# Performance work log

Hardware: AMD Instinct MI355X
Metric: run time of the kernel (lower is better)

Reference implementation:

```python
import jax, jax.numpy as jnp
import numpy as np

N = 100000
E = 1600000
IN_DIM = 128
OUT_DIM = 64


def setup_inputs() -> dict:
    key = jax.random.key(0)
    k_h, k_ei, k_ew, k_W, k_a = jax.random.split(key, 5)
    h = jax.random.normal(k_h, (N, IN_DIM), dtype=jnp.float32)
    edge_index = jax.random.randint(k_ei, (2, E), 0, N, dtype=jnp.int64)
    edge_weight = jax.random.uniform(k_ew, (E,), dtype=jnp.float32)
    # nn.Linear weights (Kaiming-uniform-ish scale)
    W = jax.random.uniform(k_W, (OUT_DIM, IN_DIM), dtype=jnp.float32,
                           minval=-1.0, maxval=1.0) / np.sqrt(IN_DIM)
    a = jax.random.uniform(k_a, (2 * OUT_DIM,), dtype=jnp.float32,
                           minval=-1.0, maxval=1.0) / np.sqrt(2 * OUT_DIM)
    return {"h": h, "edge_index": edge_index, "edge_weight": edge_weight,
            "W": W, "a": a}


def reference(h, edge_index, edge_weight, W, a):
    # Faithful translation of _GATConvSparse.forward (inference; dropout = identity).
    n = h.shape[0]
    src, dst = edge_index[0], edge_index[1]
    Wh = h @ W.T                                  # (N, out_dim)
    d = Wh.shape[1]
    # a(cat([Wh[src], Wh[dst]])) == Wh[src] @ a[:d] + Wh[dst] @ a[d:]
    alpha = Wh[src] @ a[:d] + Wh[dst] @ a[d:]     # (E,)
    alpha = alpha * edge_weight
    # Buggy-but-faithful 'softmax': segment-sum raw scores onto dst nodes...
    alpha_node = jax.ops.segment_sum(alpha, dst, num_segments=n)   # (N,)
    alpha_exp = jnp.exp(alpha_node - alpha_node.max())             # (N,)
    # ...then normalize per-edge exp(src) by sum of exp(src) over each dst segment.
    denom = jax.ops.segment_sum(alpha_exp[src], dst, num_segments=n)  # (N,)
    alpha_norm = alpha_exp[src] / (denom[dst] + 1e-9)              # (E,)
    out = jax.ops.segment_sum(alpha_norm[:, None] * Wh[src], dst,
                              num_segments=n)                      # (N, out_dim)
    return jax.nn.elu(out)
```

## Files before the change

### kernel.cpp

```cpp
#include <hip/hip_runtime.h>
#include <math.h>

#define Nn 100000
#define Ee 1600000
#define IND 128
#define OUTD 64
#define DPB 64
#define NB 1563
#define CAP 1536
#define GB 1563
#define EB_BLOCKS 391
#define AFIX 1048576.0f

using bf16x8 = __attribute__((ext_vector_type(8))) short;
using f32x4 = __attribute__((ext_vector_type(4))) float;

__device__ __forceinline__ unsigned short f2bf(float f) {
    unsigned u = __float_as_uint(f);
    u = u + 0x7FFFu + ((u >> 16) & 1u);
    return (unsigned short)(u >> 16);
}
__device__ __forceinline__ float bf2f(unsigned short h) {
    return __uint_as_float(((unsigned)h) << 16);
}

__device__ __forceinline__ bool probe64(const void* __restrict__ ei) {
    const long long* p = (const long long*)ei;
    bool ok = true;
#pragma unroll
    for (int i = 0; i < 8; ++i) {
        long long v = p[i];
        ok = ok && (v >= 0 && v < Nn);
    }
    return ok;
}

__device__ __forceinline__ void load_edge(const void* ei, int e, bool is64,
                                          int& s, int& d) {
    if (is64) {
        const long long* p = (const long long*)ei;
        s = (int)p[e];
        d = (int)p[Ee + e];
    } else {
        const int* p = (const int*)ei;
        s = p[e];
        d = p[Ee + e];
    }
}

__device__ __forceinline__ int load_dst(const void* ei, int e, bool is64) {
    if (is64) return (int)((const long long*)ei)[Ee + e];
    return ((const int*)ei)[Ee + e];
}

__global__ __launch_bounds__(256) void k_fused(
    const float* __restrict__ h, const float* __restrict__ W,
    const float* __restrict__ a, unsigned short* __restrict__ Whb,
    float* __restrict__ s1, float* __restrict__ s2,
    const void* __restrict__ ei, int* __restrict__ bcount) {
    __shared__ unsigned short Ash[64][136];
    __shared__ unsigned short Wsh[64][136];
    __shared__ float al[2 * OUTD];
    int bid = blockIdx.x;
    int t = threadIdx.x;

    if (bid < GB) {
        int R = bid * 64;
        for (int i = t; i < 2048; i += 256) {
            float4 v = ((const float4*)W)[i];
            int r = i >> 5, c = (i & 31) << 2;
            unsigned lo = (unsigned)f2bf(v.x) | ((unsigned)f2bf(v.y) << 16);
            unsigned hi = (unsigned)f2bf(v.z) | ((unsigned)f2bf(v.w) << 16);
            *(uint2*)&Wsh[r][c] = make_uint2(lo, hi);
        }
        if (t < 32) ((float4*)al)[t] = ((const float4*)a)[t];
        for (int i = t; i < 2048; i += 256) {
            int r = i >> 5, c = (i & 31) << 2;
            int n = R + r;
            float4 v = make_float4(0.f, 0.f, 0.f, 0.f);
            if (n < Nn) v = ((const float4*)(h + (size_t)n * IND))[i & 31];
            unsigned lo = (unsigned)f2bf(v.x) | ((unsigned)f2bf(v.y) << 16);
            unsigned hi = (unsigned)f2bf(v.z) | ((unsigned)f2bf(v.w) << 16);
            *(uint2*)&Ash[r][c] = make_uint2(lo, hi);
        }
        __syncthreads();

        int w = t >> 6, l = t & 63;
        int li = l & 15, lg = l >> 4;
        f32x4 acc[4];
#pragma unroll
        for (int nt = 0; nt < 4; ++nt) acc[nt] = (f32x4){0.f, 0.f, 0.f, 0.f};
#pragma unroll
        for (int kk = 0; kk < 4; ++kk) {
            bf16x8 af = *(const bf16x8*)&Ash[w * 16 + li][kk * 32 + lg * 8];
#pragma unroll
            for (int nt = 0; nt < 4; ++nt) {
                bf16x8 bf = *(const bf16x8*)&Wsh[nt * 16 + li][kk * 32 + lg * 8];
                acc[nt] = __builtin_amdgcn_mfma_f32_16x16x32_bf16(af, bf,
                                                                  acc[nt],
                                                                  0, 0, 0);
            }
        }
        float p1[4] = {0.f, 0.f, 0.f, 0.f};
        float p2[4] = {0.f, 0.f, 0.f, 0.f};
#pragma unroll
        for (int nt = 0; nt < 4; ++nt) {
            float a1v = al[nt * 16 + li];
            float a2v = al[OUTD + nt * 16 + li];
#pragma unroll
            for (int r = 0; r < 4; ++r) {
                float v = acc[nt][r];
                p1[r] += v * a1v;
                p2[r] += v * a2v;
                int row = R + w * 16 + lg * 4 + r;
                if (row < Nn)
                    Whb[(size_t)row * OUTD + nt * 16 + li] = f2bf(v);
            }
        }
#pragma unroll
        for (int r = 0; r < 4; ++r) {
#pragma unroll
            for (int m = 1; m < 16; m <<= 1) {
                p1[r] += __shfl_xor(p1[r], m, 64);
                p2[r] += __shfl_xor(p2[r], m, 64);
            }
        }
        if (li < 4) {
            int row = R + w * 16 + lg * 4 + li;
            if (row < Nn) {
                s1[row] = p1[li];
                s2[row] = p2[li];
            }
        }
    } else {
        int* cnt = (int*)&Ash[0][0];
        for (int i = t; i < NB; i += 256) cnt[i] = 0;
        __syncthreads();
        bool is64 = probe64(ei);
        int base = (bid - GB) * 4096;
#pragma unroll
        for (int i = 0; i < 16; ++i) {
            int e = base + i * 256 + t;
            if (e < Ee) atomicAdd(&cnt[load_dst(ei, e, is64) >> 6], 1);
        }
        __syncthreads();
        for (int i = t; i < NB; i += 256) {
            int c = cnt[i];
            if (c) atomicAdd(bcount + i, c);
        }
    }
}

__global__ __launch_bounds__(1024) void k_scan(
    const int* __restrict__ bcount, int* __restrict__ boff,
    int* __restrict__ bcursor) {
    __shared__ int sd[1024];
    int t = threadIdx.x;
    int i0 = 2 * t, i1 = 2 * t + 1;
    int v0 = (i0 < NB) ? bcount[i0] : 0;
    int v1 = (i1 < NB) ? bcount[i1] : 0;
    int pair = v0 + v1;
    sd[t] = pair;
    __syncthreads();
    for (int off = 1; off < 1024; off <<= 1) {
        int add = (t >= off) ? sd[t - off] : 0;
        __syncthreads();
        sd[t] += add;
        __syncthreads();
    }
    int excl = sd[t] - pair;
    if (i0 < NB) {
        boff[i0] = excl;
        bcursor[i0] = excl;
    }
    if (i1 < NB) {
        boff[i1] = excl + v0;
        bcursor[i1] = excl + v0;
    }
    if (t == 0) boff[NB] = Ee;
}

__global__ __launch_bounds__(512) void k_binscatter(
    const void* __restrict__ ei, const float* __restrict__ ew,
    const float* __restrict__ s1, const float* __restrict__ s2,
    int* __restrict__ bcursor, uint2* __restrict__ bins) {
    __shared__ int cnt[NB];
    __shared__ int gbase[NB];
    for (int i = threadIdx.x; i < NB; i += 512) cnt[i] = 0;
    __syncthreads();
    bool is64 = probe64(ei);
    int base = blockIdx.x * 4096;
    unsigned rx[8];
    int ryi[8];
    int rb[8];
    int rk[8];
#pragma unroll
    for (int i = 0; i < 8; ++i) {
        int e = base + i * 512 + threadIdx.x;
        rb[i] = -1;
        rx[i] = 0;
        ryi[i] = 0;
        rk[i] = 0;
        if (e < Ee) {
            int s, d;
            load_edge(ei, e, is64, s, d);
            float alpha = (s1[s] + s2[d]) * ew[e];
            ryi[i] = (int)rintf(alpha * AFIX);
            int b = d >> 6;
            rb[i] = b;
            rk[i] = atomicAdd(&cnt[b], 1);
            rx[i] = (unsigned)s | ((unsigned)(d & 63) << 17);
        }
    }
    __syncthreads();
    for (int i = threadIdx.x; i < NB; i += 512) {
        int c = cnt[i];
        if (c) gbase[i] = atomicAdd(bcursor + i, c);
    }
    __syncthreads();
#pragma unroll
    for (int i = 0; i < 8; ++i) {
        if (rb[i] >= 0) {
            bins[gbase[rb[i]] + rk[i]] = make_uint2(rx[i], (unsigned)ryi[i]);
        }
    }
}

__global__ __launch_bounds__(256) void k_balpha(
    const uint2* __restrict__ bins, const int* __restrict__ boff,
    float* __restrict__ ae) {
    __shared__ int anl[DPB];
    int b = blockIdx.x;
    int t = threadIdx.x;
    if (t < DPB) anl[t] = 0;
    __syncthreads();
    int e0 = boff[b], e1 = boff[b + 1];
    for (int k = e0 + t; k < e1; k += 256) {
        uint2 r = bins[k];
        atomicAdd(&anl[r.x >> 17], (int)r.y);
    }
    __syncthreads();
    if (t < DPB) {
        int n = b * DPB + t;
        if (n < Nn) ae[n] = expf((float)anl[t] * (1.f / AFIX));
    }
}

#define AGG_BODY(NR)                                                         \
    {                                                                        \
        uint2 rr[NR];                                                        \
        unsigned ww[NR];                                                     \
        _Pragma("unroll") for (int j = 0; j < NR; ++j)                       \
            rr[j] = lrec[k + 2 * j + half];                                  \
        _Pragma("unroll") for (int j = 0; j < NR; ++j)                       \
            ww[j] = whb32[(rr[j].x & 0x1FFFF) * 32 + hl];                    \
        _Pragma("unroll") for (int j = 0; j < NR; ++j) {                     \
            float aa = __uint_as_float(rr[j].y);                             \
            acc.x += aa * __uint_as_float(ww[j] << 16);                      \
            acc.y += aa * __uint_as_float(ww[j] & 0xFFFF0000u);              \
            den += aa;                                                       \
        }                                                                    \
    }

__global__ __launch_bounds__(512, 8) void k_agg(
    const uint2* __restrict__ bins, const int* __restrict__ boff,
    const float* __restrict__ ae, const unsigned short* __restrict__ Whb,
    float* __restrict__ out) {
    __shared__ uint2 lrec[CAP];
    __shared__ int cnt[DPB];
    __shared__ int sbase[DPB];
    int b = blockIdx.x;
    int t = threadIdx.x;
    int lane = t & 63;
    int wave = t >> 6;
    int half = lane >> 5;
    int hl = lane & 31;
    int e0 = boff[b], e1 = boff[b + 1];
    int total = e1 - e0;
    const unsigned* whb32 = (const unsigned*)Whb;

    if (t < DPB) cnt[t] = 0;
    __syncthreads();

    if (total <= CAP) {
        unsigned su[CAP / 512];
        float sa[CAP / 512];
        int srk[CAP / 512];
#pragma unroll
        for (int i = 0; i < CAP / 512; ++i) {
            int k = e0 + i * 512 + t;
            srk[i] = -1;
            su[i] = 0;
            sa[i] = 0.f;
            if (k < e1) {
                uint2 r = bins[k];
                srk[i] = atomicAdd(&cnt[r.x >> 17], 1);
                su[i] = r.x;
                sa[i] = ae[r.x & 0x1FFFF];
            }
        }
        __syncthreads();
        if (t < DPB) {
            int v = cnt[t];
#pragma unroll
            for (int d = 1; d < DPB; d <<= 1) {
                int u = __shfl_up(v, d, 64);
                if (t >= d) v += u;
            }
            sbase[t] = v;
        }
        __syncthreads();
#pragma unroll
        for (int i = 0; i < CAP / 512; ++i) {
            if (srk[i] >= 0) {
                int dloc = su[i] >> 17;
                int pos = sbase[dloc] - cnt[dloc] + srk[i];
                lrec[pos] = make_uint2(su[i], __float_as_uint(sa[i]));
            }
        }
        __syncthreads();

        for (int d = wave * 8; d < wave * 8 + 8; ++d) {
            int k1 = sbase[d];
            int k = k1 - cnt[d];
            float2 acc = make_float2(0.f, 0.f);
            float den = 0.f;
            for (; k + 15 < k1; k += 16) AGG_BODY(8);
            for (; k + 7 < k1; k += 8) AGG_BODY(4);
            for (; k + 1 < k1; k += 2) AGG_BODY(1);
            if (k < k1) {
                uint2 rA = lrec[k];
                unsigned wA = whb32[(rA.x & 0x1FFFF) * 32 + hl];
                float aA = half ? 0.f : __uint_as_float(rA.y);
                acc.x += aA * __uint_as_float(wA << 16);
                acc.y += aA * __uint_as_float(wA & 0xFFFF0000u);
                den += aA;
            }
            float ax = acc.x + __shfl_xor(acc.x, 32, 64);
            float ay = acc.y + __shfl_xor(acc.y, 32, 64);
            float dn = den + __shfl_xor(den, 32, 64);
            if (half == 0) {
                int n = b * DPB + d;
                if (n < Nn) {
                    float inv = 1.f / (dn + 1e-9f);
                    float vx = ax * inv;
                    float vy = ay * inv;
                    vx = vx > 0.f ? vx : expm1f(vx);
                    vy = vy > 0.f ? vy : expm1f(vy);
                    *(float2*)&out[(size_t)n * OUTD + hl * 2] =
                        make_float2(vx, vy);
                }
            }
        }
    } else {
        for (int j = 0; j < 8; ++j) {
            int dloc = wave * 8 + j;
            int n = b * DPB + dloc;
            if (n >= Nn) continue;
            float aa = 0.f, dd = 0.f;
            for (int k = e0; k < e1; ++k) {
                uint2 r = bins[k];
                if ((int)(r.x >> 17) == dloc) {
                    int s = r.x & 0x1FFFF;
                    float a = ae[s];
                    aa += a * bf2f(Whb[(size_t)s * OUTD + lane]);
                    dd += a;
                }
            }
            float v = aa / (dd + 1e-9f);
            v = v > 0.f ? v : expm1f(v);
            out[(size_t)n * OUTD + lane] = v;
        }
    }
}

extern "C" void kernel_launch(void* const* d_in, const int* in_sizes, int n_in,
                              void* d_out, int out_size, void* d_ws,
                              size_t ws_size, hipStream_t stream) {
    const float* h = (const float*)d_in[0];
    const void* ei = d_in[1];
    const float* ew = (const float*)d_in[2];
    const float* W = (const float*)d_in[3];
    const float* a = (const float*)d_in[4];
    float* out = (float*)d_out;

    unsigned short* Whb = (unsigned short*)d_ws;
    float* s1 = (float*)(Whb + (size_t)Nn * OUTD);
    float* s2 = s1 + Nn;
    float* ae = s2 + Nn;
    int* bcount = (int*)(ae + Nn);
    int* boff = bcount + 2048;
    int* bcursor = boff + 2048;
    uint2* bins = (uint2*)(bcursor + 2048);

    hipMemsetAsync(bcount, 0, 2048 * sizeof(int), stream);

    k_fused<<<GB + EB_BLOCKS, 256, 0, stream>>>(h, W, a, Whb, s1, s2, ei,
                                                bcount);
    k_scan<<<1, 1024, 0, stream>>>(bcount, boff, bcursor);
    k_binscatter<<<EB_BLOCKS, 512, 0, stream>>>(ei, ew, s1, s2, bcursor, bins);
    k_balpha<<<NB, 256, 0, stream>>>(bins, boff, ae);
    k_agg<<<NB, 512, 0, stream>>>(bins, boff, ae, Whb, out);
}
```

Measured before the change: 117.1 us.

## Accumulate alpha via global atomics, shrink bin records to 32 bits

The per-edge fixed-point alpha is now accumulated into a per-node global array with atomicAdd during binning, instead of being stored in each bin record and reduced by a separate pass. That removes k_balpha's re-read of all bins and halves the bin record to one packed 32-bit word, with the source index pre-shifted into a byte offset. A light elementwise exp kernel replaces the binned reduction. The cost is 1.6M global integer atomics onto random nodes. The aggregation kernel also uses pointer-stepped LDS reads and has its occupancy hint lowered from 8 to 4.

```diff
diff --git a/kernel.cpp b/kernel.cpp
--- a/kernel.cpp
+++ b/kernel.cpp
@@ -183,7 +183,8 @@
 __global__ __launch_bounds__(512) void k_binscatter(
     const void* __restrict__ ei, const float* __restrict__ ew,
     const float* __restrict__ s1, const float* __restrict__ s2,
-    int* __restrict__ bcursor, uint2* __restrict__ bins) {
+    int* __restrict__ bcursor, unsigned* __restrict__ bins,
+    int* __restrict__ an) {
     __shared__ int cnt[NB];
     __shared__ int gbase[NB];
     for (int i = threadIdx.x; i < NB; i += 512) cnt[i] = 0;
@@ -191,7 +192,6 @@
     bool is64 = probe64(ei);
     int base = blockIdx.x * 4096;
     unsigned rx[8];
-    int ryi[8];
     int rb[8];
     int rk[8];
 #pragma unroll
@@ -199,17 +199,16 @@
         int e = base + i * 512 + threadIdx.x;
         rb[i] = -1;
         rx[i] = 0;
-        ryi[i] = 0;
         rk[i] = 0;
         if (e < Ee) {
             int s, d;
             load_edge(ei, e, is64, s, d);
             float alpha = (s1[s] + s2[d]) * ew[e];
-            ryi[i] = (int)rintf(alpha * AFIX);
+            atomicAdd(an + d, (int)rintf(alpha * AFIX));
             int b = d >> 6;
             rb[i] = b;
             rk[i] = atomicAdd(&cnt[b], 1);
-            rx[i] = (unsigned)s | ((unsigned)(d & 63) << 17);
+            rx[i] = ((unsigned)s << 7) | ((unsigned)(d & 63) << 24);
         }
     }
     __syncthreads();
@@ -220,30 +219,14 @@
     __syncthreads();
 #pragma unroll
     for (int i = 0; i < 8; ++i) {
-        if (rb[i] >= 0) {
-            bins[gbase[rb[i]] + rk[i]] = make_uint2(rx[i], (unsigned)ryi[i]);
-        }
-    }
-}
-
-__global__ __launch_bounds__(256) void k_balpha(
-    const uint2* __restrict__ bins, const int* __restrict__ boff,
-    float* __restrict__ ae) {
-    __shared__ int anl[DPB];
-    int b = blockIdx.x;
-    int t = threadIdx.x;
-    if (t < DPB) anl[t] = 0;
-    __syncthreads();
-    int e0 = boff[b], e1 = boff[b + 1];
-    for (int k = e0 + t; k < e1; k += 256) {
-        uint2 r = bins[k];
-        atomicAdd(&anl[r.x >> 17], (int)r.y);
-    }
-    __syncthreads();
-    if (t < DPB) {
-        int n = b * DPB + t;
-        if (n < Nn) ae[n] = expf((float)anl[t] * (1.f / AFIX));
-    }
+        if (rb[i] >= 0) bins[gbase[rb[i]] + rk[i]] = rx[i];
+    }
+}
+
+__global__ __launch_bounds__(256) void k_exp(const int* __restrict__ an,
+                                             float* __restrict__ ae) {
+    int n = blockIdx.x * 256 + threadIdx.x;
+    if (n < Nn) ae[n] = expf((float)an[n] * (1.f / AFIX));
 }
 
 #define AGG_BODY(NR)                                                         \
@@ -251,19 +234,20 @@
         uint2 rr[NR];                                                        \
         unsigned ww[NR];                                                     \
         _Pragma("unroll") for (int j = 0; j < NR; ++j)                       \
-            rr[j] = lrec[k + 2 * j + half];                                  \
+            rr[j] = lp[2 * j];                                               \
         _Pragma("unroll") for (int j = 0; j < NR; ++j)                       \
-            ww[j] = whb32[(rr[j].x & 0x1FFFF) * 32 + hl];                    \
+            ww[j] = *(const unsigned*)(whbB + (rr[j].x + hl4));              \
         _Pragma("unroll") for (int j = 0; j < NR; ++j) {                     \
             float aa = __uint_as_float(rr[j].y);                             \
             acc.x += aa * __uint_as_float(ww[j] << 16);                      \
             acc.y += aa * __uint_as_float(ww[j] & 0xFFFF0000u);              \
             den += aa;                                                       \
         }                                                                    \
-    }
-
-__global__ __launch_bounds__(512, 8) void k_agg(
-    const uint2* __restrict__ bins, const int* __restrict__ boff,
+        lp += 2 * NR;                                                        \
+    }
+
+__global__ __launch_bounds__(512, 4) void k_agg(
+    const unsigned* __restrict__ bins, const int* __restrict__ boff,
     const float* __restrict__ ae, const unsigned short* __restrict__ Whb,
     float* __restrict__ out) {
     __shared__ uint2 lrec[CAP];
@@ -275,9 +259,10 @@
     int wave = t >> 6;
     int half = lane >> 5;
     int hl = lane & 31;
+    unsigned hl4 = (unsigned)hl << 2;
     int e0 = boff[b], e1 = boff[b + 1];
     int total = e1 - e0;
-    const unsigned* whb32 = (const unsigned*)Whb;
+    const char* whbB = (const char*)Whb;
 
     if (t < DPB) cnt[t] = 0;
     __syncthreads();
@@ -293,10 +278,10 @@
             su[i] = 0;
             sa[i] = 0.f;
             if (k < e1) {
-                uint2 r = bins[k];
-                srk[i] = atomicAdd(&cnt[r.x >> 17], 1);
-                su[i] = r.x;
-                sa[i] = ae[r.x & 0x1FFFF];
+                unsigned u = bins[k];
+                srk[i] = atomicAdd(&cnt[u >> 24], 1);
+                su[i] = u;
+                sa[i] = ae[(u >> 7) & 0x1FFFF];
             }
         }
         __syncthreads();
@@ -313,9 +298,10 @@
 #pragma unroll
         for (int i = 0; i < CAP / 512; ++i) {
             if (srk[i] >= 0) {
-                int dloc = su[i] >> 17;
+                int dloc = su[i] >> 24;
                 int pos = sbase[dloc] - cnt[dloc] + srk[i];
-                lrec[pos] = make_uint2(su[i], __float_as_uint(sa[i]));
+                lrec[pos] = make_uint2(su[i] & 0xFFFFFFu,
+                                       __float_as_uint(sa[i]));
             }
         }
         __syncthreads();
@@ -323,6 +309,7 @@
         for (int d = wave * 8; d < wave * 8 + 8; ++d) {
             int k1 = sbase[d];
             int k = k1 - cnt[d];
+            const uint2* lp = lrec + k + half;
             float2 acc = make_float2(0.f, 0.f);
             float den = 0.f;
             for (; k + 15 < k1; k += 16) AGG_BODY(8);
@@ -330,7 +317,7 @@
             for (; k + 1 < k1; k += 2) AGG_BODY(1);
             if (k < k1) {
                 uint2 rA = lrec[k];
-                unsigned wA = whb32[(rA.x & 0x1FFFF) * 32 + hl];
+                unsigned wA = *(const unsigned*)(whbB + (rA.x + hl4));
                 float aA = half ? 0.f : __uint_as_float(rA.y);
                 acc.x += aA * __uint_as_float(wA << 16);
                 acc.y += aA * __uint_as_float(wA & 0xFFFF0000u);
@@ -359,9 +346,9 @@
             if (n >= Nn) continue;
             float aa = 0.f, dd = 0.f;
             for (int k = e0; k < e1; ++k) {
-                uint2 r = bins[k];
-                if ((int)(r.x >> 17) == dloc) {
-                    int s = r.x & 0x1FFFF;
+                unsigned u = bins[k];
+                if ((int)(u >> 24) == dloc) {
+                    int s = (int)((u >> 7) & 0x1FFFF);
                     float a = ae[s];
                     aa += a * bf2f(Whb[(size_t)s * OUTD + lane]);
                     dd += a;
@@ -388,17 +375,19 @@
     float* s1 = (float*)(Whb + (size_t)Nn * OUTD);
     float* s2 = s1 + Nn;
     float* ae = s2 + Nn;
-    int* bcount = (int*)(ae + Nn);
+    int* an = (int*)(ae + Nn);
+    int* bcount = an + Nn;
     int* boff = bcount + 2048;
     int* bcursor = boff + 2048;
-    uint2* bins = (uint2*)(bcursor + 2048);
-
-    hipMemsetAsync(bcount, 0, 2048 * sizeof(int), stream);
+    unsigned* bins = (unsigned*)(bcursor + 2048);
+
+    hipMemsetAsync(an, 0, (Nn + 2048) * sizeof(int), stream);
 
     k_fused<<<GB + EB_BLOCKS, 256, 0, stream>>>(h, W, a, Whb, s1, s2, ei,
                                                 bcount);
     k_scan<<<1, 1024, 0, stream>>>(bcount, boff, bcursor);
-    k_binscatter<<<EB_BLOCKS, 512, 0, stream>>>(ei, ew, s1, s2, bcursor, bins);
-    k_balpha<<<NB, 256, 0, stream>>>(bins, boff, ae);
+    k_binscatter<<<EB_BLOCKS, 512, 0, stream>>>(ei, ew, s1, s2, bcursor,
+                                                bins, an);
+    k_exp<<<(Nn + 255) / 256, 256, 0, stream>>>(an, ae);
     k_agg<<<NB, 512, 0, stream>>>(bins, boff, ae, Whb, out);
 }
```

Measured after the change: 164.6 us. +40.6%, slower.
